# Optimization experiments

Measured on AMD Instinct MI355X. Metric: run time of the kernel, lower is better.

Reference implementation:

```python
import jax, jax.numpy as jnp
import numpy as np

N, V, J, NB = 512, 3889, 35, 20
PARENTS = np.array([0, 0, 1, 2, 3, 4, 5, 6, 7, 8, 9, 6, 11, 12, 13, 6, 15, 16, 17, 18,
                    16, 20, 21, 22, 23, 16, 25, 26, 27, 28, 29, 30, 16, 1, 1], dtype=np.int32)


def _rodrigues(theta):
    # theta: [M,3] axis-angle -> [M,3,3] rotation matrices (batch_rodrigues)
    angle = jnp.sqrt(jnp.sum(theta * theta, axis=1, keepdims=True) + 1e-8)  # [M,1]
    r = theta / angle                                                        # [M,3]
    c = jnp.cos(angle)[..., None]                                            # [M,1,1]
    s = jnp.sin(angle)[..., None]
    rr = r[:, :, None] * r[:, None, :]                                       # [M,3,3]
    z = jnp.zeros_like(r[:, 0])
    K = jnp.stack([z, -r[:, 2], r[:, 1],
                   r[:, 2], z, -r[:, 0],
                   -r[:, 1], r[:, 0], z], axis=1).reshape(-1, 3, 3)
    eye = jnp.eye(3, dtype=theta.dtype)
    return c * eye + (1.0 - c) * rr + s * K


def _make_A(R, t):
    # R: [N,3,3], t: [N,3] -> homogeneous [N,4,4]
    n = R.shape[0]
    top = jnp.concatenate([R, t[:, :, None]], axis=2)                        # [N,3,4]
    bot = jnp.broadcast_to(jnp.array([0.0, 0.0, 0.0, 1.0], R.dtype), (n, 1, 4))
    return jnp.concatenate([top, bot], axis=1)


def _global_rigid(Rs, Jp, scales, parents):
    # Rs: [N,35,3,3], Jp: [N,35,3], scales: [N,35,3] (diag scale factors)
    # diag(s_par)^-1 @ R @ diag(s) == R * s[col] / s_par[row]
    results = [_make_A(Rs[:, 0], Jp[:, 0])]
    for i in range(1, len(parents)):  # fixed 35-joint kinematic tree
        p = int(parents[i])
        j_here = Jp[:, i] - Jp[:, p]
        rot_new = Rs[:, i] * (scales[:, i][:, None, :] / scales[:, p][:, :, None])
        results.append(results[p] @ _make_A(rot_new, j_here))
    results = jnp.stack(results, axis=1)                                     # [N,35,4,4]
    new_J = results[:, :, :3, 3]
    # A = results - pad(results @ [J;0]) : subtract rest-pose bone from last column
    init_bone = jnp.einsum('njab,njb->nja', results[:, :, :, :3], Jp)        # [N,35,4]
    A = results - jnp.pad(init_bone[..., None], ((0, 0), (0, 0), (0, 0), (3, 0)))
    return new_J, A


def reference(beta, theta, betas_extra, deform_verts, trans, v_template,
              shapedirs, posedirs, J_regressor, weights, parents):
    par = np.asarray(jax.device_get(parents))
    n = beta.shape[0]
    v_shaped = v_template + deform_verts + (beta @ shapedirs).reshape(n, V, 3)
    Jp = jnp.einsum('nvc,vj->njc', v_shaped, J_regressor)                    # [N,35,3]
    Rs = _rodrigues(theta.reshape(n * J, 3)).reshape(n, J, 3, 3)
    pose_feature = (Rs[:, 1:] - jnp.eye(3, dtype=Rs.dtype)).reshape(n, 306)
    v_posed = (pose_feature @ posedirs).reshape(n, V, 3) + v_shaped
    scales = betas_extra.reshape(n, J, 3)
    _, A = _global_rigid(Rs, Jp, scales, par)
    T = jnp.einsum('vj,njab->nvab', weights, A)                              # [N,V,4,4] LBS blend
    v_h = jnp.concatenate([v_posed, jnp.ones((n, V, 1), v_posed.dtype)], axis=2)
    verts = jnp.einsum('nvab,nvb->nva', T, v_h)[..., :3] + trans[:, None, :]
    joints = jnp.einsum('nvc,vj->njc', verts, J_regressor)
    return verts, joints, Rs


def setup_inputs() -> dict:
    key = jax.random.key(0)
    ks = jax.random.split(key, 10)
    beta = 0.5 * jax.random.normal(ks[0], (N, NB), jnp.float32)
    theta = 0.2 * jax.random.normal(ks[1], (N, J * 3), jnp.float32)
    betas_extra = jnp.exp(0.1 * jax.random.normal(ks[2], (N, J * 3), jnp.float32))  # positive scales ~1
    deform_verts = 0.01 * jax.random.normal(ks[3], (N, V, 3), jnp.float32)
    trans = jax.random.normal(ks[4], (N, 3), jnp.float32)
    v_template = jax.random.normal(ks[5], (V, 3), jnp.float32)
    shapedirs = 0.01 * jax.random.normal(ks[6], (NB, V * 3), jnp.float32)
    posedirs = 0.01 * jax.random.normal(ks[7], (306, V * 3), jnp.float32)
    Jr = jax.random.uniform(ks[8], (V, J), jnp.float32)
    J_regressor = Jr / jnp.sum(Jr, axis=0, keepdims=True)   # columns sum to 1
    Wt = jax.random.uniform(ks[9], (V, J), jnp.float32)
    weights = Wt / jnp.sum(Wt, axis=1, keepdims=True)       # rows sum to 1 (skinning weights)
    return {"beta": beta, "theta": theta, "betas_extra": betas_extra,
            "deform_verts": deform_verts, "trans": trans, "v_template": v_template,
            "shapedirs": shapedirs, "posedirs": posedirs, "J_regressor": J_regressor,
            "weights": weights, "parents": jnp.asarray(PARENTS)}
```

## Files before the change

kernel.cpp:

```cpp
#include <hip/hip_runtime.h>

#define N_   512
#define V_   3889
#define V3   11667
#define J_   35
#define NB_  20
#define PF_K 306
#define KP2  352
#define KS2  11
#define EP2  11776
#define VP   3904
#define JRROWS 36
#define JCP  112
#define KB_  23
#define ECH  512
#define PLN  57344

typedef __attribute__((ext_vector_type(8))) short short8;
typedef __attribute__((ext_vector_type(4))) float f32x4;

__constant__ int c_parents[J_] = {0,0,1,2,3,4,5,6,7,8,9,6,11,12,13,6,15,16,17,18,
                                  16,20,21,22,23,16,25,26,27,28,29,30,16,1,1};

static __device__ __forceinline__ unsigned short f2bf(float x) {
  union { float f; unsigned int u; } v; v.f = x;
  unsigned int r = v.u + 0x7FFF + ((v.u >> 16) & 1);
  return (unsigned short)(r >> 16);
}

#define PA_JRT 549
#define PA_WTS 245
#define PA_PD  2024
#define PA_JB  644
#define PA_BLOCKS (PA_JRT + PA_WTS + PA_PD + PA_JB)
__global__ __launch_bounds__(256) void k_prep_a(
    const float* __restrict__ Jr,  const float* __restrict__ wts,
    const float* __restrict__ pd,  const float* __restrict__ sd,
    float* __restrict__ JrT, unsigned short* __restrict__ wtsB,
    unsigned short* __restrict__ pdT, unsigned short* __restrict__ JrBigT) {
  int b = blockIdx.x;
  int t = threadIdx.x;
  if (b < PA_JRT) {
    int idx = b * 256 + t;
    if (idx >= JRROWS * VP) return;
    int j = idx / VP, v = idx - j * VP;
    JrT[idx] = (j < J_ && v < V_) ? Jr[v * J_ + j] : 0.f;
  } else if (b < PA_JRT + PA_WTS) {
    int bb = b - PA_JRT;
    int v   = bb * 16 + (t >> 4);
    int jk0 = (t & 15) * 4;
    unsigned short pk[4];
#pragma unroll
    for (int i = 0; i < 4; ++i) {
      int j = jk0 + i;
      float x = (v < V_ && j < J_) ? wts[(size_t)v * J_ + j] : 0.f;
      pk[i] = f2bf(x);
    }
    *(unsigned long long*)(wtsB + (size_t)v * 64 + jk0) = *(unsigned long long*)pk;
  } else if (b < PA_JRT + PA_WTS + PA_PD) {
    int pp = b - (PA_JRT + PA_WTS);
    int ec = pp % 184, o4 = pp / 184;
    int e  = ec * 64 + (t & 63);
    int oc = o4 * 4 + (t >> 6);
    int k0 = oc * 8;
    bool ev = e < V3;
    union { unsigned short u[8]; short8 s; } pk;
#pragma unroll
    for (int ii = 0; ii < 8; ++ii) {
      int k = k0 + ii;
      float x = 0.f;
      if (ev && k < PF_K)            x = pd[(size_t)k * V3 + e];
      else if (ev && k < PF_K + NB_) x = sd[(size_t)(k - PF_K) * V3 + e];
      pk.u[ii] = f2bf(x);
    }
    size_t dst = (size_t)(e >> 4) * 704 + (size_t)(oc >> 2) * 64
               + (oc & 3) * 16 + (e & 15);
    *(short8*)(pdT + dst * 8) = pk.s;
  } else {
    int o = (b - (PA_JRT + PA_WTS + PA_PD)) * 256 + t;
    int jc = o / 1472;
    int oc = o - jc * 1472;
    int eo = oc * 8;
    int jj = jc / 3, cc = jc - jj * 3;
    union { unsigned short u[8]; short8 s; } pk;
#pragma unroll
    for (int i = 0; i < 8; ++i) {
      int e = eo + i;
      int v = e / 3, ce = e - v * 3;
      float x = (jc < 105 && e < V3 && ce == cc) ? Jr[v * J_ + jj] : 0.f;
      pk.u[i] = f2bf(x);
    }
    size_t dst = (size_t)(oc >> 2) * 448 + (size_t)(jc >> 4) * 64
               + (oc & 3) * 16 + (jc & 15);
    *(short8*)(JrBigT + dst * 8) = pk.s;
  }
}

#define JRJG 9
__global__ __launch_bounds__(512) void k_jp84(
    const float* __restrict__ JrT, const float* __restrict__ vt,
    const float* __restrict__ sd,  float* __restrict__ vtsdJr) {
  __shared__ float part[8][27];
  int b = blockIdx.x;
  int t = threadIdx.x;
  int lane = t & 63, w = t >> 6;
  int jg = w & 3, vh = w >> 2;
  int j0 = jg * JRJG;
  const float* jrb = JrT + (size_t)j0 * VP;

  int d = b >> 3, ch = b & 7;
  const float* s0 = (d == 0) ? vt : sd + (size_t)(d - 1) * V3;
  int c0 = ch * 2 + vh, cn = 1;
  bool tail = false;
  if (ch == 7 && vh == 1) { cn = 0; tail = true; }

  float acc[JRJG][3];
#pragma unroll
  for (int jj = 0; jj < JRJG; ++jj)
#pragma unroll
    for (int cc = 0; cc < 3; ++cc) acc[jj][cc] = 0.f;

  for (int i = 0; i < cn; ++i) {
    int v = (c0 + i) * 256 + lane * 4;
    f32x4 jr4[JRJG];
#pragma unroll
    for (int jj = 0; jj < JRJG; ++jj)
      jr4[jj] = *(const f32x4*)&jrb[(size_t)jj * VP + v];
    const float* dp = s0 + 3 * v;
    f32x4 da = *(const f32x4*)(dp);
    f32x4 db = *(const f32x4*)(dp + 4);
    f32x4 dc = *(const f32x4*)(dp + 8);
#pragma unroll
    for (int jj = 0; jj < JRJG; ++jj) {
      acc[jj][0] += jr4[jj][0]*da[0] + jr4[jj][1]*da[3] + jr4[jj][2]*db[2] + jr4[jj][3]*dc[1];
      acc[jj][1] += jr4[jj][0]*da[1] + jr4[jj][1]*db[0] + jr4[jj][2]*db[3] + jr4[jj][3]*dc[2];
      acc[jj][2] += jr4[jj][0]*da[2] + jr4[jj][1]*db[1] + jr4[jj][2]*dc[0] + jr4[jj][3]*dc[3];
    }
  }

  if (tail) {
    int v = 15 * 256 + lane * 4;
#pragma unroll
    for (int k = 0; k < 4; ++k) {
      int vv = v + k;
      if (vv < V_) {
        float dx = s0[3*vv], dy = s0[3*vv+1], dz = s0[3*vv+2];
#pragma unroll
        for (int jj = 0; jj < JRJG; ++jj) {
          float jr = jrb[(size_t)jj * VP + vv];
          acc[jj][0] += jr * dx; acc[jj][1] += jr * dy; acc[jj][2] += jr * dz;
        }
      }
    }
  }

#pragma unroll
  for (int jj = 0; jj < JRJG; ++jj)
#pragma unroll
    for (int cc = 0; cc < 3; ++cc) {
      float v = acc[jj][cc];
#pragma unroll
      for (int off = 32; off > 0; off >>= 1)
        v += __shfl_down(v, off, 64);
      if (lane == 0) part[w][jj * 3 + cc] = v;
    }
  __syncthreads();

  if (t < 108) {
    int g = t / 27, idx = t % 27;
    int j = g * JRJG + idx / 3;
    if (j < J_)
      atomicAdd(&vtsdJr[(b >> 3) * 105 + j * 3 + idx % 3],
                part[g][idx] + part[g + 4][idx]);
  }
}

__global__ __launch_bounds__(64) void k_jrgemm(
    const float* __restrict__ X, const unsigned short* __restrict__ JrBigT,
    float* __restrict__ planes) {
  int lane = threadIdx.x;
  int q = lane >> 4, c = lane & 15;
  int n = blockIdx.x * 16 + c;
  int kb = blockIdx.y;
  int e0 = kb * ECH;
  const float* xr = X + (size_t)n * V3;
  const short8* Ap = (const short8*)JrBigT;

  f32x4 acc[7];
#pragma unroll
  for (int tt = 0; tt < 7; ++tt) acc[tt] = (f32x4){0.f, 0.f, 0.f, 0.f};

  bool safe = (e0 + ECH <= V3);
  if (safe) {
#pragma unroll
    for (int ks = 0; ks < ECH / 32; ++ks) {
      int eb = e0 + ks * 32 + q * 8;
      f32x4 x0 = *(const f32x4*)(xr + eb);
      f32x4 x1 = *(const f32x4*)(xr + eb + 4);
      union { unsigned short u[8]; short8 s; } bq;
#pragma unroll
      for (int i = 0; i < 4; ++i) { bq.u[i] = f2bf(x0[i]); bq.u[4 + i] = f2bf(x1[i]); }
#pragma unroll
      for (int tt = 0; tt < 7; ++tt) {
        short8 a = Ap[(size_t)(kb * 16 + ks) * 448 + tt * 64 + lane];
        acc[tt] = __builtin_amdgcn_mfma_f32_16x16x32_bf16(a, bq.s, acc[tt], 0, 0, 0);
      }
    }
  } else {
#pragma unroll
    for (int ks = 0; ks < ECH / 32; ++ks) {
      int eb = e0 + ks * 32 + q * 8;
      union { unsigned short u[8]; short8 s; } bq;
#pragma unroll
      for (int i = 0; i < 8; ++i) {
        int e = eb + i;
        float x = (e < V3) ? xr[e] : 0.f;
        bq.u[i] = f2bf(x);
      }
#pragma unroll
      for (int tt = 0; tt < 7; ++tt) {
        short8 a = Ap[(size_t)(kb * 16 + ks) * 448 + tt * 64 + lane];
        acc[tt] = __builtin_amdgcn_mfma_f32_16x16x32_bf16(a, bq.s, acc[tt], 0, 0, 0);
      }
    }
  }

  float* pl = planes + (size_t)kb * PLN + (size_t)n * JCP;
#pragma unroll
  for (int tt = 0; tt < 7; ++tt)
    *(f32x4*)(pl + tt * 16 + q * 4) = acc[tt];
}

__global__ __launch_bounds__(256) void k_fold(
    const float* __restrict__ planes, float* __restrict__ dst) {
  int g = blockIdx.x * 256 + threadIdx.x;
  int n = g / 105, jc = g - n * 105;
  float s = 0.f;
#pragma unroll
  for (int kb = 0; kb < KB_; ++kb)
    s += planes[(size_t)kb * PLN + n * JCP + jc];
  dst[g] = s;
}

__global__ __launch_bounds__(64) void k_chain_rod(
    const float* __restrict__ theta, const float* __restrict__ JpRaw,
    const float* __restrict__ vtsdJr,
    const float* __restrict__ se,    const float* __restrict__ trans,
    const float* __restrict__ beta,
    float* __restrict__ Rs_out, unsigned short* __restrict__ pfA,
    unsigned short* __restrict__ AwB) {
  __shared__ float loc[J_][12];
  __shared__ float res[J_][12];
  __shared__ float Jp_s[J_][3];
  int l = threadIdx.x;
  int n = blockIdx.x;
  int mt = n >> 4, m = n & 15;

  float r[9];
  if (l < J_) {
    int j = l;
    const float* th = theta + n * (J_ * 3) + j * 3;
    float t0 = th[0], t1 = th[1], t2 = th[2];
    float angle = sqrtf(t0 * t0 + t1 * t1 + t2 * t2 + 1e-8f);
    float inv = 1.0f / angle;
    float r0 = t0 * inv, r1 = t1 * inv, r2 = t2 * inv;
    float s, c;
    sincosf(angle, &s, &c);
    float omc = 1.0f - c;
    r[0] = c + omc * r0 * r0;      r[1] = omc * r0 * r1 - s * r2;  r[2] = omc * r0 * r2 + s * r1;
    r[3] = omc * r1 * r0 + s * r2; r[4] = c + omc * r1 * r1;       r[5] = omc * r1 * r2 - s * r0;
    r[6] = omc * r2 * r0 - s * r1; r[7] = omc * r2 * r1 + s * r0;  r[8] = c + omc * r2 * r2;

    float* ro = Rs_out + (size_t)n * (J_ * 9) + j * 9;
#pragma unroll
    for (int k = 0; k < 9; ++k) ro[k] = r[k];
    if (j > 0) {
#pragma unroll
      for (int kk = 0; kk < 9; ++kk) {
        int k = (j - 1) * 9 + kk;
        float v = r[kk] - ((kk == 0 || kk == 4 || kk == 8) ? 1.0f : 0.0f);
        size_t idx = ((((size_t)mt * KS2 + (k >> 5)) * 4 + ((k >> 3) & 3)) * 16 + m) * 8 + (k & 7);
        pfA[idx] = f2bf(v);
      }
    }
    const float* bn = beta + n * NB_;
#pragma unroll
    for (int cc = 0; cc < 3; ++cc) {
      int jc = j * 3 + cc;
      float val = JpRaw[n * 105 + jc] + vtsdJr[jc];
#pragma unroll
      for (int bb = 0; bb < NB_; ++bb)
        val += bn[bb] * vtsdJr[(1 + bb) * 105 + jc];
      Jp_s[j][cc] = val;
    }
  } else {
    unsigned short* An = AwB + (size_t)n * 16 * 64 + l;
#pragma unroll
    for (int d = 0; d < 16; ++d) An[d * 64] = 0;
    if (l < 55) {
      int k = PF_K + (l - 35);
      size_t idx = ((((size_t)mt * KS2 + (k >> 5)) * 4 + ((k >> 3) & 3)) * 16 + m) * 8 + (k & 7);
      pfA[idx] = f2bf(beta[n * NB_ + (l - 35)]);
    } else {
      for (int k = PF_K + NB_ + (l - 55); k < KP2; k += 9) {
        size_t idx = ((((size_t)mt * KS2 + (k >> 5)) * 4 + ((k >> 3) & 3)) * 16 + m) * 8 + (k & 7);
        pfA[idx] = 0;
      }
    }
  }

  if (l < J_) {
    int j = l;
    if (j == 0) {
#pragma unroll
      for (int rr = 0; rr < 3; ++rr) {
        loc[0][rr * 4 + 0] = r[rr * 3 + 0];
        loc[0][rr * 4 + 1] = r[rr * 3 + 1];
        loc[0][rr * 4 + 2] = r[rr * 3 + 2];
        loc[0][rr * 4 + 3] = Jp_s[0][rr];
      }
#pragma unroll
      for (int k = 0; k < 12; ++k) res[0][k] = loc[0][k];
    } else {
      int p = c_parents[j];
      float si[3], sp[3], jh[3];
#pragma unroll
      for (int cidx = 0; cidx < 3; ++cidx) {
        si[cidx] = se[n * 105 + j * 3 + cidx];
        sp[cidx] = se[n * 105 + p * 3 + cidx];
        jh[cidx] = Jp_s[j][cidx] - Jp_s[p][cidx];
      }
#pragma unroll
      for (int rr = 0; rr < 3; ++rr) {
        float invp = 1.0f / sp[rr];
        loc[j][rr * 4 + 0] = r[rr * 3 + 0] * si[0] * invp;
        loc[j][rr * 4 + 1] = r[rr * 3 + 1] * si[1] * invp;
        loc[j][rr * 4 + 2] = r[rr * 3 + 2] * si[2] * invp;
        loc[j][rr * 4 + 3] = jh[rr];
      }
    }
  }

  for (int i = 1; i < J_; ++i) {
    if (l < 12) {
      int p = c_parents[i];
      int rr = l >> 2, cc = l & 3;
      float acc = (cc == 3) ? res[p][rr * 4 + 3] : 0.f;
#pragma unroll
      for (int k = 0; k < 3; ++k)
        acc += res[p][rr * 4 + k] * loc[i][k * 4 + cc];
      res[i][l] = acc;
    }
  }

  if (l < J_) {
    int j = l;
    float jx = Jp_s[j][0];
    float jy = Jp_s[j][1];
    float jz = Jp_s[j][2];
    unsigned short* An = AwB + (size_t)n * 16 * 64 + j;
#pragma unroll
    for (int rr = 0; rr < 3; ++rr) {
      float a0 = res[j][rr * 4 + 0];
      float a1 = res[j][rr * 4 + 1];
      float a2 = res[j][rr * 4 + 2];
      float a3 = res[j][rr * 4 + 3] - (a0 * jx + a1 * jy + a2 * jz)
               + trans[n * 3 + rr];
      An[(rr * 4 + 0) * 64] = f2bf(a0);
      An[(rr * 4 + 1) * 64] = f2bf(a1);
      An[(rr * 4 + 2) * 64] = f2bf(a2);
      An[(rr * 4 + 3) * 64] = f2bf(a3);
    }
  }
}

#define LSTR 242
__global__ __launch_bounds__(256) void k_vposed_skin(
    const unsigned short* __restrict__ pfA, const unsigned short* __restrict__ pdT,
    const unsigned short* __restrict__ AwB, const unsigned short* __restrict__ wtsB,
    const float* __restrict__ vt, const float* __restrict__ deform,
    float* __restrict__ verts) {
  __shared__ float lds[64 * LSTR];
  int t = threadIdx.x;
  int wv = t >> 6, lane = t & 63;
  int q = lane >> 4, col = lane & 15;
  int bx = blockIdx.x, by = blockIdx.y;
  int mtg0 = by * 4;
  int ebase = bx * 240 + wv * 64;
  int e16b = ebase >> 4;

  const short8* Ap = (const short8*)pfA;
  const short8* Bp = (const short8*)pdT;

  f32x4 acc[4][4];
#pragma unroll
  for (int mt = 0; mt < 4; ++mt)
#pragma unroll
    for (int et = 0; et < 4; ++et) acc[mt][et] = (f32x4){0.f, 0.f, 0.f, 0.f};

#pragma unroll
  for (int ks = 0; ks < KS2; ++ks) {
    short8 a[4];
#pragma unroll
    for (int mt = 0; mt < 4; ++mt)
      a[mt] = Ap[(((mtg0 + mt) * KS2 + ks) * 4 + q) * 16 + col];
    short8 b[4];
#pragma unroll
    for (int et = 0; et < 4; ++et)
      b[et] = Bp[(size_t)(e16b + et) * 704 + ks * 64 + lane];
#pragma unroll
    for (int mt = 0; mt < 4; ++mt)
#pragma unroll
      for (int et = 0; et < 4; ++et)
        acc[mt][et] = __builtin_amdgcn_mfma_f32_16x16x32_bf16(a[mt], b[et], acc[mt][et], 0, 0, 0);
  }

#pragma unroll
  for (int et = 0; et < 4; ++et) {
    int e_loc = wv * 64 + et * 16 + col;
    int e = bx * 240 + e_loc;
    bool ev = (e < V3) && (e_loc < 240);
    float vte = ev ? vt[e] : 0.f;
#pragma unroll
    for (int mt = 0; mt < 4; ++mt) {
#pragma unroll
      for (int r = 0; r < 4; ++r) {
        int n_loc = mt * 16 + q * 4 + r;
        if (ev) {
          int n = by * 64 + n_loc;
          float df = deform[(size_t)n * V3 + e];
          lds[n_loc * LSTR + e_loc] = acc[mt][et][r] + vte + df;
        }
      }
    }
  }
  __syncthreads();

  short8 bw0[5], bw1[5];
#pragma unroll
  for (int v5 = 0; v5 < 5; ++v5) {
    int v = bx * 80 + v5 * 16 + col;
    const short8* Wp = (const short8*)(wtsB + (size_t)v * 64);
    bw0[v5] = Wp[q];
    bw1[v5] = Wp[4 + q];
  }
#pragma unroll 2
  for (int ni = 0; ni < 16; ++ni) {
    int n_loc = wv * 16 + ni;
    int n = by * 64 + n_loc;
    const short8* Aq = (const short8*)(AwB + ((size_t)n * 16 + col) * 64);
    short8 a0 = Aq[q];
    short8 a1 = Aq[4 + q];
#pragma unroll
    for (int v5 = 0; v5 < 5; ++v5) {
      f32x4 s = (f32x4){0.f, 0.f, 0.f, 0.f};
      s = __builtin_amdgcn_mfma_f32_16x16x32_bf16(a0, bw0[v5], s, 0, 0, 0);
      s = __builtin_amdgcn_mfma_f32_16x16x32_bf16(a1, bw1[v5], s, 0, 0, 0);
      int vl = v5 * 16 + col;
      int v = bx * 80 + vl;
      if (v < V_ && q < 3) {
        float x = lds[n_loc * LSTR + 3 * vl + 0];
        float y = lds[n_loc * LSTR + 3 * vl + 1];
        float z = lds[n_loc * LSTR + 3 * vl + 2];
        verts[(size_t)n * V3 + 3 * v + q] = s[0] * x + s[1] * y + s[2] * z + s[3];
      }
    }
  }
}

extern "C" void kernel_launch(void* const* d_in, const int* in_sizes, int n_in,
                              void* d_out, int out_size, void* d_ws, size_t ws_size,
                              hipStream_t stream) {
  const float* beta   = (const float*)d_in[0];
  const float* theta  = (const float*)d_in[1];
  const float* se     = (const float*)d_in[2];
  const float* deform = (const float*)d_in[3];
  const float* trans  = (const float*)d_in[4];
  const float* vt     = (const float*)d_in[5];
  const float* sd     = (const float*)d_in[6];
  const float* pd     = (const float*)d_in[7];
  const float* Jr     = (const float*)d_in[8];
  const float* wts    = (const float*)d_in[9];

  float* out    = (float*)d_out;
  float* verts  = out;
  float* joints = out + (size_t)N_ * V3;
  float* Rs     = joints + (size_t)N_ * 105;

  char* w = (char*)d_ws;
  unsigned short* pdT    = (unsigned short*)w;
  unsigned short* pfA    = (unsigned short*)(w + 8290304);
  float* planes = (float*)(w + 8650752);
  float* JpRawF = (float*)(w + 13926400);
  unsigned short* AwB    = (unsigned short*)(w + 14141440);
  float* JrT    = (float*)(w + 15190016);
  unsigned short* wtsB   = (unsigned short*)(w + 15752192);
  unsigned short* JrBigT = (unsigned short*)(w + 16253952);
  float* vtsdJr = (float*)(w + 18891776);

  hipMemsetAsync(vtsdJr, 0, 21 * 105 * sizeof(float), stream);
  k_prep_a<<<PA_BLOCKS, 256, 0, stream>>>(Jr, wts, pd, sd, JrT, wtsB, pdT, JrBigT);
  k_jp84<<<168, 512, 0, stream>>>(JrT, vt, sd, vtsdJr);
  k_jrgemm<<<dim3(32, KB_), 64, 0, stream>>>(deform, JrBigT, planes);
  k_fold<<<210, 256, 0, stream>>>(planes, JpRawF);
  k_chain_rod<<<N_, 64, 0, stream>>>(theta, JpRawF, vtsdJr, se, trans, beta,
                                     Rs, pfA, AwB);
  k_vposed_skin<<<dim3(49, 8), 256, 0, stream>>>(pfA, pdT, AwB, wtsB, vt, deform, verts);
  k_jrgemm<<<dim3(32, KB_), 64, 0, stream>>>(verts, JrBigT, planes);
  k_fold<<<210, 256, 0, stream>>>(planes, joints);
}
```

Before: 206.8 us.

## Fold template/shapedir joint regression into bf16 MFMA jrgemm and vectorize skin epilogue

Removes the separate fp32 k_jp84 kernel, its JrT transpose, and the memset. Template and shapedir rows are now staged as extra input rows (21 real, padded to 32) and pushed through the existing bf16 MFMA joint-regressor GEMM alongside deform. The vposed_skin epilogue first writes the accumulators to LDS, then adds vt and deform with vectorized float4 loads, and the LDS stride is padded. This cuts two launches and the uncoalesced scalar loads, but the template/shapedir regression now runs in bf16 rather than fp32.

```diff
diff --git a/kernel.cpp b/kernel.cpp
--- a/kernel.cpp
+++ b/kernel.cpp
@@ -9,12 +9,11 @@
 #define KP2  352
 #define KS2  11
 #define EP2  11776
-#define VP   3904
-#define JRROWS 36
 #define JCP  112
 #define KB_  23
 #define ECH  512
-#define PLN  57344
+#define XROWS 544
+#define PLN  60928
 
 typedef __attribute__((ext_vector_type(8))) short short8;
 typedef __attribute__((ext_vector_type(4))) float f32x4;
@@ -28,26 +27,21 @@
   return (unsigned short)(r >> 16);
 }
 
-#define PA_JRT 549
 #define PA_WTS 245
 #define PA_PD  2024
 #define PA_JB  644
-#define PA_BLOCKS (PA_JRT + PA_WTS + PA_PD + PA_JB)
+#define PA_VS  365
+#define PA_BLOCKS (PA_WTS + PA_PD + PA_JB + PA_VS)
 __global__ __launch_bounds__(256) void k_prep_a(
     const float* __restrict__ Jr,  const float* __restrict__ wts,
     const float* __restrict__ pd,  const float* __restrict__ sd,
-    float* __restrict__ JrT, unsigned short* __restrict__ wtsB,
-    unsigned short* __restrict__ pdT, unsigned short* __restrict__ JrBigT) {
+    const float* __restrict__ vt,
+    unsigned short* __restrict__ wtsB, unsigned short* __restrict__ pdT,
+    unsigned short* __restrict__ JrBigT, float* __restrict__ vtsd) {
   int b = blockIdx.x;
   int t = threadIdx.x;
-  if (b < PA_JRT) {
-    int idx = b * 256 + t;
-    if (idx >= JRROWS * VP) return;
-    int j = idx / VP, v = idx - j * VP;
-    JrT[idx] = (j < J_ && v < V_) ? Jr[v * J_ + j] : 0.f;
-  } else if (b < PA_JRT + PA_WTS) {
-    int bb = b - PA_JRT;
-    int v   = bb * 16 + (t >> 4);
+  if (b < PA_WTS) {
+    int v   = b * 16 + (t >> 4);
     int jk0 = (t & 15) * 4;
     unsigned short pk[4];
 #pragma unroll
@@ -57,8 +51,8 @@
       pk[i] = f2bf(x);
     }
     *(unsigned long long*)(wtsB + (size_t)v * 64 + jk0) = *(unsigned long long*)pk;
-  } else if (b < PA_JRT + PA_WTS + PA_PD) {
-    int pp = b - (PA_JRT + PA_WTS);
+  } else if (b < PA_WTS + PA_PD) {
+    int pp = b - PA_WTS;
     int ec = pp % 184, o4 = pp / 184;
     int e  = ec * 64 + (t & 63);
     int oc = o4 * 4 + (t >> 6);
@@ -76,8 +70,8 @@
     size_t dst = (size_t)(e >> 4) * 704 + (size_t)(oc >> 2) * 64
                + (oc & 3) * 16 + (e & 15);
     *(short8*)(pdT + dst * 8) = pk.s;
-  } else {
-    int o = (b - (PA_JRT + PA_WTS + PA_PD)) * 256 + t;
+  } else if (b < PA_WTS + PA_PD + PA_JB) {
+    int o = (b - (PA_WTS + PA_PD)) * 256 + t;
     int jc = o / 1472;
     int oc = o - jc * 1472;
     int eo = oc * 8;
@@ -93,97 +87,32 @@
     size_t dst = (size_t)(oc >> 2) * 448 + (size_t)(jc >> 4) * 64
                + (oc & 3) * 16 + (jc & 15);
     *(short8*)(JrBigT + dst * 8) = pk.s;
-  }
-}
-
-#define JRJG 9
-__global__ __launch_bounds__(512) void k_jp84(
-    const float* __restrict__ JrT, const float* __restrict__ vt,
-    const float* __restrict__ sd,  float* __restrict__ vtsdJr) {
-  __shared__ float part[8][27];
-  int b = blockIdx.x;
-  int t = threadIdx.x;
-  int lane = t & 63, w = t >> 6;
-  int jg = w & 3, vh = w >> 2;
-  int j0 = jg * JRJG;
-  const float* jrb = JrT + (size_t)j0 * VP;
-
-  int d = b >> 3, ch = b & 7;
-  const float* s0 = (d == 0) ? vt : sd + (size_t)(d - 1) * V3;
-  int c0 = ch * 2 + vh, cn = 1;
-  bool tail = false;
-  if (ch == 7 && vh == 1) { cn = 0; tail = true; }
-
-  float acc[JRJG][3];
-#pragma unroll
-  for (int jj = 0; jj < JRJG; ++jj)
-#pragma unroll
-    for (int cc = 0; cc < 3; ++cc) acc[jj][cc] = 0.f;
-
-  for (int i = 0; i < cn; ++i) {
-    int v = (c0 + i) * 256 + lane * 4;
-    f32x4 jr4[JRJG];
-#pragma unroll
-    for (int jj = 0; jj < JRJG; ++jj)
-      jr4[jj] = *(const f32x4*)&jrb[(size_t)jj * VP + v];
-    const float* dp = s0 + 3 * v;
-    f32x4 da = *(const f32x4*)(dp);
-    f32x4 db = *(const f32x4*)(dp + 4);
-    f32x4 dc = *(const f32x4*)(dp + 8);
-#pragma unroll
-    for (int jj = 0; jj < JRJG; ++jj) {
-      acc[jj][0] += jr4[jj][0]*da[0] + jr4[jj][1]*da[3] + jr4[jj][2]*db[2] + jr4[jj][3]*dc[1];
-      acc[jj][1] += jr4[jj][0]*da[1] + jr4[jj][1]*db[0] + jr4[jj][2]*db[3] + jr4[jj][3]*dc[2];
-      acc[jj][2] += jr4[jj][0]*da[2] + jr4[jj][1]*db[1] + jr4[jj][2]*dc[0] + jr4[jj][3]*dc[3];
-    }
-  }
-
-  if (tail) {
-    int v = 15 * 256 + lane * 4;
+  } else {
+    int f0 = (b - (PA_WTS + PA_PD + PA_JB)) * 1024 + t * 4;
 #pragma unroll
     for (int k = 0; k < 4; ++k) {
-      int vv = v + k;
-      if (vv < V_) {
-        float dx = s0[3*vv], dy = s0[3*vv+1], dz = s0[3*vv+2];
-#pragma unroll
-        for (int jj = 0; jj < JRJG; ++jj) {
-          float jr = jrb[(size_t)jj * VP + vv];
-          acc[jj][0] += jr * dx; acc[jj][1] += jr * dy; acc[jj][2] += jr * dz;
-        }
-      }
-    }
-  }
-
-#pragma unroll
-  for (int jj = 0; jj < JRJG; ++jj)
-#pragma unroll
-    for (int cc = 0; cc < 3; ++cc) {
-      float v = acc[jj][cc];
-#pragma unroll
-      for (int off = 32; off > 0; off >>= 1)
-        v += __shfl_down(v, off, 64);
-      if (lane == 0) part[w][jj * 3 + cc] = v;
-    }
-  __syncthreads();
-
-  if (t < 108) {
-    int g = t / 27, idx = t % 27;
-    int j = g * JRJG + idx / 3;
-    if (j < J_)
-      atomicAdd(&vtsdJr[(b >> 3) * 105 + j * 3 + idx % 3],
-                part[g][idx] + part[g + 4][idx]);
+      int f = f0 + k;
+      if (f < 32 * V3) {
+        int row = f / V3, col = f - row * V3;
+        float x = 0.f;
+        if (row == 0) x = vt[col];
+        else if (row <= NB_) x = sd[(size_t)(row - 1) * V3 + col];
+        vtsd[f] = x;
+      }
+    }
   }
 }
 
 __global__ __launch_bounds__(64) void k_jrgemm(
-    const float* __restrict__ X, const unsigned short* __restrict__ JrBigT,
-    float* __restrict__ planes) {
+    const float* __restrict__ X, const float* __restrict__ X2,
+    const unsigned short* __restrict__ JrBigT, float* __restrict__ planes) {
   int lane = threadIdx.x;
   int q = lane >> 4, c = lane & 15;
-  int n = blockIdx.x * 16 + c;
+  int row = blockIdx.x * 16 + c;
   int kb = blockIdx.y;
   int e0 = kb * ECH;
-  const float* xr = X + (size_t)n * V3;
+  const float* xr = (row < N_) ? X + (size_t)row * V3
+                               : X2 + (size_t)(row - N_) * V3;
   const short8* Ap = (const short8*)JrBigT;
 
   f32x4 acc[7];
@@ -225,21 +154,24 @@
     }
   }
 
-  float* pl = planes + (size_t)kb * PLN + (size_t)n * JCP;
+  float* pl = planes + (size_t)kb * PLN + (size_t)row * JCP;
 #pragma unroll
   for (int tt = 0; tt < 7; ++tt)
     *(f32x4*)(pl + tt * 16 + q * 4) = acc[tt];
 }
 
 __global__ __launch_bounds__(256) void k_fold(
-    const float* __restrict__ planes, float* __restrict__ dst) {
+    const float* __restrict__ planes, float* __restrict__ dst,
+    float* __restrict__ dst2, int total) {
   int g = blockIdx.x * 256 + threadIdx.x;
+  if (g >= total) return;
   int n = g / 105, jc = g - n * 105;
   float s = 0.f;
 #pragma unroll
   for (int kb = 0; kb < KB_; ++kb)
     s += planes[(size_t)kb * PLN + n * JCP + jc];
-  dst[g] = s;
+  if (n < N_) dst[n * 105 + jc] = s;
+  else dst2[(n - N_) * 105 + jc] = s;
 }
 
 __global__ __launch_bounds__(64) void k_chain_rod(
@@ -374,7 +306,7 @@
   }
 }
 
-#define LSTR 242
+#define LSTR 244
 __global__ __launch_bounds__(256) void k_vposed_skin(
     const unsigned short* __restrict__ pfA, const unsigned short* __restrict__ pdT,
     const unsigned short* __restrict__ AwB, const unsigned short* __restrict__ wtsB,
@@ -418,23 +350,40 @@
 #pragma unroll
   for (int et = 0; et < 4; ++et) {
     int e_loc = wv * 64 + et * 16 + col;
-    int e = bx * 240 + e_loc;
-    bool ev = (e < V3) && (e_loc < 240);
-    float vte = ev ? vt[e] : 0.f;
-#pragma unroll
-    for (int mt = 0; mt < 4; ++mt) {
-#pragma unroll
-      for (int r = 0; r < 4; ++r) {
-        int n_loc = mt * 16 + q * 4 + r;
-        if (ev) {
-          int n = by * 64 + n_loc;
-          float df = deform[(size_t)n * V3 + e];
-          lds[n_loc * LSTR + e_loc] = acc[mt][et][r] + vte + df;
-        }
-      }
+    if (e_loc < 240) {
+#pragma unroll
+      for (int mt = 0; mt < 4; ++mt)
+#pragma unroll
+        for (int r = 0; r < 4; ++r)
+          lds[(mt * 16 + q * 4 + r) * LSTR + e_loc] = acc[mt][et][r];
     }
   }
   __syncthreads();
+
+  if (lane < 60) {
+    int e = bx * 240 + lane * 4;
+    bool full = (e + 4 <= V3);
+    f32x4 vt4 = (f32x4){0.f, 0.f, 0.f, 0.f};
+    if (full) vt4 = *(const f32x4*)(vt + e);
+    else {
+#pragma unroll
+      for (int k2 = 0; k2 < 4; ++k2) if (e + k2 < V3) vt4[k2] = vt[e + k2];
+    }
+#pragma unroll
+    for (int i = 0; i < 16; ++i) {
+      int n_loc = wv * 16 + i;
+      int n = by * 64 + n_loc;
+      const float* dp = deform + (size_t)n * V3 + e;
+      f32x4 d4 = (f32x4){0.f, 0.f, 0.f, 0.f};
+      if (full) d4 = *(const f32x4*)dp;
+      else {
+#pragma unroll
+        for (int k2 = 0; k2 < 4; ++k2) if (e + k2 < V3) d4[k2] = dp[k2];
+      }
+      f32x4* lp = (f32x4*)&lds[n_loc * LSTR + lane * 4];
+      *lp = *lp + vt4 + d4;
+    }
+  }
 
   short8 bw0[5], bw1[5];
 #pragma unroll
@@ -491,21 +440,20 @@
   unsigned short* pdT    = (unsigned short*)w;
   unsigned short* pfA    = (unsigned short*)(w + 8290304);
   float* planes = (float*)(w + 8650752);
-  float* JpRawF = (float*)(w + 13926400);
-  unsigned short* AwB    = (unsigned short*)(w + 14141440);
-  float* JrT    = (float*)(w + 15190016);
-  unsigned short* wtsB   = (unsigned short*)(w + 15752192);
-  unsigned short* JrBigT = (unsigned short*)(w + 16253952);
-  float* vtsdJr = (float*)(w + 18891776);
-
-  hipMemsetAsync(vtsdJr, 0, 21 * 105 * sizeof(float), stream);
-  k_prep_a<<<PA_BLOCKS, 256, 0, stream>>>(Jr, wts, pd, sd, JrT, wtsB, pdT, JrBigT);
-  k_jp84<<<168, 512, 0, stream>>>(JrT, vt, sd, vtsdJr);
-  k_jrgemm<<<dim3(32, KB_), 64, 0, stream>>>(deform, JrBigT, planes);
-  k_fold<<<210, 256, 0, stream>>>(planes, JpRawF);
+  float* JpRawF = (float*)(w + 14256128);
+  unsigned short* AwB    = (unsigned short*)(w + 14471168);
+  unsigned short* wtsB   = (unsigned short*)(w + 15519744);
+  unsigned short* JrBigT = (unsigned short*)(w + 16021504);
+  float* vtsd   = (float*)(w + 18659328);
+  float* vtsdJr = (float*)(w + 20152704);
+
+  k_prep_a<<<PA_BLOCKS, 256, 0, stream>>>(Jr, wts, pd, sd, vt,
+                                          wtsB, pdT, JrBigT, vtsd);
+  k_jrgemm<<<dim3(34, KB_), 64, 0, stream>>>(deform, vtsd, JrBigT, planes);
+  k_fold<<<219, 256, 0, stream>>>(planes, JpRawF, vtsdJr, 533 * 105);
   k_chain_rod<<<N_, 64, 0, stream>>>(theta, JpRawF, vtsdJr, se, trans, beta,
                                      Rs, pfA, AwB);
   k_vposed_skin<<<dim3(49, 8), 256, 0, stream>>>(pfA, pdT, AwB, wtsB, vt, deform, verts);
-  k_jrgemm<<<dim3(32, KB_), 64, 0, stream>>>(verts, JrBigT, planes);
-  k_fold<<<210, 256, 0, stream>>>(planes, joints);
-}
+  k_jrgemm<<<dim3(32, KB_), 64, 0, stream>>>(verts, verts, JrBigT, planes);
+  k_fold<<<210, 256, 0, stream>>>(planes, joints, vtsdJr, N_ * 105);
+}
```

Result: faster. 200.6 us (-3.0%).
